# Optimization experiments

Measured on AMD Instinct MI355X. Metric: run time of the kernel, lower is better.

## Reference

```python
import jax, jax.numpy as jnp
import numpy as np

B, F, V, E, A = 8192, 39, 1_000_000, 16, 16  # batch, fields, vocab, embed, attn


def setup_inputs() -> dict:
    key = jax.random.key(0)
    ks = jax.random.split(key, 9)
    return {
        "feat_index": jax.random.randint(ks[0], (B, F), 0, V),
        "feat_value": jax.random.uniform(ks[1], (B, F), dtype=jnp.float32),
        "first_order_weights": jax.random.normal(ks[2], (V, 1), dtype=jnp.float32) * 0.01,
        "emb_table": jax.random.normal(ks[3], (V, E), dtype=jnp.float32) * 0.01,
        "bias": jax.random.normal(ks[4], (1,), dtype=jnp.float32),
        "attention_w": jax.random.normal(ks[5], (E, A), dtype=jnp.float32) * 0.1,
        "attention_b": jax.random.normal(ks[6], (A,), dtype=jnp.float32) * 0.1,
        "projection_h": jax.random.normal(ks[7], (A, 1), dtype=jnp.float32) * 0.1,
        "projection_p": jax.random.normal(ks[8], (E, 1), dtype=jnp.float32) * 0.1,
    }


def reference(feat_index, feat_value, first_order_weights, emb_table, bias,
              attention_w, attention_b, projection_h, projection_p):
    fv = feat_value[..., None]                                  # [B,F,1]
    # first order: gather weights, scale by value, sum over fields
    y_first = jnp.sum(first_order_weights[feat_index] * fv, axis=1)[:, 0]  # [B]
    # embeddings scaled by feature values
    emb = emb_table[feat_index] * fv                            # [B,F,E]
    # pairwise bi-interaction over all i<j field pairs (num_pairs = F*(F-1)/2)
    iu, ju = np.triu_indices(F, k=1)
    bi = emb[:, iu, :] * emb[:, ju, :]                          # [B,P,E]
    # tiny attention MLP + softmax over pairs
    att = jax.nn.relu(jnp.einsum('bpe,ea->bpa', bi, attention_w) + attention_b)
    score = jax.nn.softmax(jnp.einsum('bpa,ao->bpo', att, projection_h), axis=1)  # [B,P,1]
    pooled = jnp.sum(score * bi, axis=1)                        # [B,E]
    aw = (pooled @ projection_p)[:, 0]                          # [B]
    y = bias + y_first + aw                                     # [B]
    return jax.nn.sigmoid(y)
```

## Files before the change

### kernel.cpp

```cpp
#include <hip/hip_runtime.h>
#include <hip/hip_fp16.h>
#include <math.h>


#define BB 8192
#define FF 39
#define PP 741
#define NT 24
#define RBYTES 48
#define SBYTES (FF * RBYTES)
#define STGB   (FF * 64)
#define CH     (FF * 4)
#define SPW    2
#define WLDS   (STGB + SBYTES)

typedef _Float16 f16x8 __attribute__((ext_vector_type(8)));
typedef _Float16 h2    __attribute__((ext_vector_type(2)));
typedef __fp16   hw2   __attribute__((ext_vector_type(2)));
typedef float    f32x4  __attribute__((ext_vector_type(4)));
typedef float    f32x16 __attribute__((ext_vector_type(16)));

struct alignas(16) PijT { unsigned v[32][NT]; };
static constexpr PijT make_pij() {
    PijT t{};
    int p = 0;
    for (int i = 0; i < FF; ++i)
        for (int j = i + 1; j < FF; ++j) {
            t.v[p & 31][p >> 5] =
                ((unsigned)(i * RBYTES) << 16) | (unsigned)(j * RBYTES);
            ++p;
        }
    return t;
}
__device__ constexpr PijT c_pij = make_pij();

static __device__ __forceinline__ h2 cvt2(float lo, float hi) {
    return __builtin_bit_cast(h2, __builtin_amdgcn_cvt_pkrtz(lo, hi));
}
static __device__ __forceinline__ h2 ash2(unsigned d) {
    return __builtin_bit_cast(h2, d);
}
static __device__ __forceinline__ float fdot2f(h2 a, h2 b, float c) {
    return __builtin_amdgcn_fdot2(__builtin_bit_cast(hw2, a),
                                  __builtin_bit_cast(hw2, b), c, false);
}
static __device__ __forceinline__ h2 relu2(h2 x) {
    const h2 zz = {(_Float16)0.f, (_Float16)0.f};
    return __builtin_elementwise_max(x, zz);
}

static __device__ __forceinline__ void gld_lds16(const void* g, void* l) {
    __builtin_amdgcn_global_load_lds(
        (const __attribute__((address_space(1))) void*)g,
        (__attribute__((address_space(3))) void*)l, 16, 0, 0);
}

__global__ __launch_bounds__(256, 4)
void afm_kernel(const int*   __restrict__ fidx,
                const float* __restrict__ fval,
                const float* __restrict__ fow,
                const float* __restrict__ emb,
                const float* __restrict__ bias,
                const float* __restrict__ aw_,
                const float* __restrict__ ab_,
                const float* __restrict__ ph_,
                const float* __restrict__ pp_,
                float*       __restrict__ out)
{
    __shared__ __align__(16) unsigned char s_all[4 * WLDS];

    const int tid  = threadIdx.x;
    const int wid  = tid >> 6;
    const int lane = tid & 63;
    const int n    = lane & 31;
    const int h    = lane >> 5;
    const int s0   = (blockIdx.x * 4 + wid) * SPW;

    unsigned char* stg = s_all + wid * WLDS;
    unsigned char* my  = stg + STGB;

    int idxA = 0, idxB = 0; float vA = 0.f, vB = 0.f;
    if (lane < FF) {
        idxA = fidx[s0 * FF + lane];
        vA   = fval[s0 * FF + lane];
        idxB = fidx[(s0 + 1) * FF + lane];
        vB   = fval[(s0 + 1) * FF + lane];
    }

    const float LOG2E = 1.44269504088896f;
    const f32x4 ph_lo = ((const f32x4*)ph_)[h];
    const f32x4 ph_hi = ((const f32x4*)ph_)[h + 2];
    const f32x4 ab_lo = ((const f32x4*)ab_)[h];
    const f32x4 ab_hi = ((const f32x4*)ab_)[h + 2];
    float t0 = 0.f, t1 = 0.f, t2 = 0.f, t3 = 0.f,
          t4 = 0.f, t5 = 0.f, t6 = 0.f, t7 = 0.f;
    if (n < 16) {
        const float* base = aw_ + (8 * h) * 16 + n;
        t0 = base[0];   t1 = base[16];  t2 = base[32];  t3 = base[48];
        t4 = base[64];  t5 = base[80];  t6 = base[96];  t7 = base[112];
    } else if (n == 16) {
        const float* base = pp_ + 8 * h;
        t0 = base[0]; t1 = base[1]; t2 = base[2]; t3 = base[3];
        t4 = base[4]; t5 = base[5]; t6 = base[6]; t7 = base[7];
    }
    unsigned po[NT];
    {
        const uint4* myp4 = (const uint4*)c_pij.v[n];
        #pragma unroll
        for (int g = 0; g < 6; ++g) {
            uint4 q = myp4[g];
            po[4 * g + 0] = q.x; po[4 * g + 1] = q.y;
            po[4 * g + 2] = q.z; po[4 * g + 3] = q.w;
        }
    }

    float foA = (lane < FF) ? fow[idxA] : 0.f;
    float foB = (lane < FF) ? fow[idxB] : 0.f;

    const int r0 = lane >> 2, r1 = (64 + lane) >> 2, r2 = (128 + lane) >> 2;
    const int cA0 = __shfl(idxA, r0), cA1 = __shfl(idxA, r1),
              cA2 = __shfl(idxA, r2);
    const int cB0 = __shfl(idxB, r0), cB1 = __shfl(idxB, r1),
              cB2 = __shfl(idxB, r2);
    const int q4 = (lane & 3) * 4;

    gld_lds16(emb + (size_t)(unsigned)cA0 * 16 + q4, stg);
    gld_lds16(emb + (size_t)(unsigned)cA1 * 16 + q4, stg + 1024);
    if (lane < CH - 128)
        gld_lds16(emb + (size_t)(unsigned)cA2 * 16 + q4, stg + 2048);

    h2 hp0 = cvt2(ph_lo[0] * LOG2E, ph_lo[1] * LOG2E);
    h2 hp1 = cvt2(ph_lo[2] * LOG2E, ph_lo[3] * LOG2E);
    h2 hp2 = cvt2(ph_hi[0] * LOG2E, ph_hi[1] * LOG2E);
    h2 hp3 = cvt2(ph_hi[2] * LOG2E, ph_hi[3] * LOG2E);

    f32x16 cinit;
    cinit[0] = ab_lo[0]; cinit[1] = ab_lo[1];
    cinit[2] = ab_lo[2]; cinit[3] = ab_lo[3];
    cinit[4] = ab_hi[0]; cinit[5] = ab_hi[1];
    cinit[6] = ab_hi[2]; cinit[7] = ab_hi[3];
    #pragma unroll
    for (int r = 8; r < 16; ++r) cinit[r] = 0.f;

    f16x8 wfrag;
    {
        union { h2 hh[4]; f16x8 v; } u;
        u.hh[0] = cvt2(t0, t1); u.hh[1] = cvt2(t2, t3);
        u.hh[2] = cvt2(t4, t5); u.hh[3] = cvt2(t6, t7);
        wfrag = u.v;
    }

    const unsigned char* bpre = my + h * 16;

    float vcur = vA, vnxt = vB;
    float fcur = foA, fnxt = foB;

    #pragma unroll 1
    for (int s = 0; s < SPW; ++s) {
        asm volatile("s_waitcnt vmcnt(0)" ::: "memory");
        __builtin_amdgcn_sched_barrier(0);

        #pragma unroll
        for (int k = 0; k < 3; ++k) {
            const int u   = 64 * k + lane;
            const int row = u >> 2, q = u & 3;
            const float v = __shfl(vcur, row);
            if (u < CH) {
                const f32x4 e = *(const f32x4*)(stg + u * 16);
                h2 a0 = cvt2(e[0] * v, e[1] * v);
                h2 a1 = cvt2(e[2] * v, e[3] * v);
                uint2 dd = make_uint2(__builtin_bit_cast(unsigned, a0),
                                      __builtin_bit_cast(unsigned, a1));
                *(uint2*)(my + row * RBYTES + q * 8) = dd;
            }
        }

        asm volatile("s_waitcnt lgkmcnt(0)" ::: "memory");
        __builtin_amdgcn_sched_barrier(0);

        if (s == 0) {
            gld_lds16(emb + (size_t)(unsigned)cB0 * 16 + q4, stg);
            gld_lds16(emb + (size_t)(unsigned)cB1 * 16 + q4, stg + 1024);
            if (lane < CH - 128)
                gld_lds16(emb + (size_t)(unsigned)cB2 * 16 + q4, stg + 2048);
        }

        float aw = 0.f;
        float z  = 0.f;

        uint4 di = *(const uint4*)(bpre + (po[0] >> 16));
        uint4 dj = *(const uint4*)(bpre + (po[0] & 0xFFFFu));

        #pragma unroll
        for (int t = 0; t < NT; ++t) {
            uint4 diN = di, djN = dj;
            if (t + 1 < NT) {
                diN = *(const uint4*)(bpre + (po[t + 1] >> 16));
                djN = *(const uint4*)(bpre + (po[t + 1] & 0xFFFFu));
            }
            h2 m0 = ash2(di.x) * ash2(dj.x);
            h2 m1 = ash2(di.y) * ash2(dj.y);
            h2 m2 = ash2(di.z) * ash2(dj.z);
            h2 m3 = ash2(di.w) * ash2(dj.w);
            union { h2 hh[4]; f16x8 v; } u;
            u.hh[0] = m0; u.hh[1] = m1; u.hh[2] = m2; u.hh[3] = m3;
            f32x16 d = __builtin_amdgcn_mfma_f32_32x32x16_f16(wfrag, u.v,
                                                              cinit, 0, 0, 0);
            h2 c0 = relu2(cvt2(d[0], d[1]));
            h2 c1 = relu2(cvt2(d[2], d[3]));
            h2 c2 = relu2(cvt2(d[4], d[5]));
            h2 c3 = relu2(cvt2(d[6], d[7]));
            float sc = fdot2f(c0, hp0,
                       fdot2f(c1, hp1,
                       fdot2f(c2, hp2,
                       fdot2f(c3, hp3, 0.f))));
            sc += __shfl_xor(sc, 32);
            float w = __builtin_amdgcn_exp2f(sc);
            if (t == NT - 1) w = (n < PP - (NT - 1) * 32) ? w : 0.f;
            z  += w;
            aw  = fmaf(w, d[8], aw);
            di = diN; dj = djN;
        }

        float fo = fcur * vcur;
        #pragma unroll
        for (int m = 1; m < 64; m <<= 1) {
            aw += __shfl_xor(aw, m);
            z  += __shfl_xor(z, m);
            fo += __shfl_xor(fo, m);
        }
        if (lane == 0) {
            float y = bias[0] + fo + 2.f * aw / z;
            out[s0 + s] = 1.f / (1.f + __expf(-y));
        }

        vcur = vnxt; fcur = fnxt;
    }
}

extern "C" void kernel_launch(void* const* d_in, const int* in_sizes, int n_in,
                              void* d_out, int out_size, void* d_ws, size_t ws_size,
                              hipStream_t stream) {
    const int*   fidx      = (const int*)  d_in[0];
    const float* fval      = (const float*)d_in[1];
    const float* fow       = (const float*)d_in[2];
    const float* emb_table = (const float*)d_in[3];
    const float* bias      = (const float*)d_in[4];
    const float* attn_w    = (const float*)d_in[5];
    const float* attn_b    = (const float*)d_in[6];
    const float* proj_h    = (const float*)d_in[7];
    const float* proj_p    = (const float*)d_in[8];
    float* out = (float*)d_out;

    afm_kernel<<<BB / (4 * SPW), 256, 0, stream>>>(fidx, fval, fow, emb_table,
                                                   bias, attn_w, attn_b,
                                                   proj_h, proj_p, out);
}
```

Baseline: 126.9 us.

## Move pair-offset table from registers to LDS and shrink blocks to two waves

The 24 per-lane pair offsets were held in registers. They are now written into a shared LDS table at kernel start and read back with a two-step-ahead prefetch inside the pair loop. Blocks shrink from four waves to two, with launch bounds raised to five blocks per CU, to cut register pressure and raise occupancy. The cost is an extra LDS read per iteration and a table fill per block. The table fill has no barrier, but each wave only reads entries it wrote itself, so the code stays correct.

```diff
diff --git a/kernel.cpp b/kernel.cpp
--- a/kernel.cpp
+++ b/kernel.cpp
@@ -13,6 +13,7 @@
 #define CH     (FF * 4)
 #define SPW    2
 #define WLDS   (STGB + SBYTES)
+#define POB    (NT * 32 * 4)
 
 typedef _Float16 f16x8 __attribute__((ext_vector_type(8)));
 typedef _Float16 h2    __attribute__((ext_vector_type(2)));
@@ -55,7 +56,7 @@
         (__attribute__((address_space(3))) void*)l, 16, 0, 0);
 }
 
-__global__ __launch_bounds__(256, 4)
+__global__ __launch_bounds__(128, 5)
 void afm_kernel(const int*   __restrict__ fidx,
                 const float* __restrict__ fval,
                 const float* __restrict__ fow,
@@ -67,17 +68,22 @@
                 const float* __restrict__ pp_,
                 float*       __restrict__ out)
 {
-    __shared__ __align__(16) unsigned char s_all[4 * WLDS];
+    __shared__ __align__(16) unsigned char s_all[POB + 2 * WLDS];
 
     const int tid  = threadIdx.x;
     const int wid  = tid >> 6;
     const int lane = tid & 63;
     const int n    = lane & 31;
     const int h    = lane >> 5;
-    const int s0   = (blockIdx.x * 4 + wid) * SPW;
-
-    unsigned char* stg = s_all + wid * WLDS;
+    const int s0   = (blockIdx.x * 2 + wid) * SPW;
+
+    unsigned*      po_lds = (unsigned*)s_all;
+    unsigned char* stg = s_all + POB + wid * WLDS;
     unsigned char* my  = stg + STGB;
+
+    #pragma unroll
+    for (int u = lane; u < NT * 32; u += 64)
+        po_lds[u] = c_pij.v[u & 31][u >> 5];
 
     int idxA = 0, idxB = 0; float vA = 0.f, vB = 0.f;
     if (lane < FF) {
@@ -103,16 +109,6 @@
         t0 = base[0]; t1 = base[1]; t2 = base[2]; t3 = base[3];
         t4 = base[4]; t5 = base[5]; t6 = base[6]; t7 = base[7];
     }
-    unsigned po[NT];
-    {
-        const uint4* myp4 = (const uint4*)c_pij.v[n];
-        #pragma unroll
-        for (int g = 0; g < 6; ++g) {
-            uint4 q = myp4[g];
-            po[4 * g + 0] = q.x; po[4 * g + 1] = q.y;
-            po[4 * g + 2] = q.z; po[4 * g + 3] = q.w;
-        }
-    }
 
     float foA = (lane < FF) ? fow[idxA] : 0.f;
     float foB = (lane < FF) ? fow[idxB] : 0.f;
@@ -188,15 +184,20 @@
         float aw = 0.f;
         float z  = 0.f;
 
-        uint4 di = *(const uint4*)(bpre + (po[0] >> 16));
-        uint4 dj = *(const uint4*)(bpre + (po[0] & 0xFFFFu));
+        unsigned po0 = po_lds[n];
+        unsigned pon = po_lds[32 + n];
+        uint4 di = *(const uint4*)(bpre + (po0 >> 16));
+        uint4 dj = *(const uint4*)(bpre + (po0 & 0xFFFFu));
 
         #pragma unroll
         for (int t = 0; t < NT; ++t) {
+            unsigned pon2 = 0;
+            if (t + 2 < NT)
+                pon2 = po_lds[(t + 2) * 32 + n];
             uint4 diN = di, djN = dj;
             if (t + 1 < NT) {
-                diN = *(const uint4*)(bpre + (po[t + 1] >> 16));
-                djN = *(const uint4*)(bpre + (po[t + 1] & 0xFFFFu));
+                diN = *(const uint4*)(bpre + (pon >> 16));
+                djN = *(const uint4*)(bpre + (pon & 0xFFFFu));
             }
             h2 m0 = ash2(di.x) * ash2(dj.x);
             h2 m1 = ash2(di.y) * ash2(dj.y);
@@ -219,7 +220,7 @@
             if (t == NT - 1) w = (n < PP - (NT - 1) * 32) ? w : 0.f;
             z  += w;
             aw  = fmaf(w, d[8], aw);
-            di = diN; dj = djN;
+            di = diN; dj = djN; pon = pon2;
         }
 
         float fo = fcur * vcur;
@@ -252,7 +253,7 @@
     const float* proj_p    = (const float*)d_in[8];
     float* out = (float*)d_out;
 
-    afm_kernel<<<BB / (4 * SPW), 256, 0, stream>>>(fidx, fval, fow, emb_table,
+    afm_kernel<<<BB / (2 * SPW), 128, 0, stream>>>(fidx, fval, fow, emb_table,
                                                    bias, attn_w, attn_b,
                                                    proj_h, proj_p, out);
 }
```

Result: slower. 131.0 us (+3.3%).
